# Kernel tuning notes

Measured on AMD Instinct MI355X. Metric: run time of the kernel, lower is better.

## Reference

```python
import jax, jax.numpy as jnp
import numpy as np

N_IN = 1024
N_OUT = 1024
BATCH = 8192
N_GRID = 10  # grid_points = linspace(-1, 1, 10); 9 segments
LN_EPS = 1e-5


def setup_inputs() -> dict:
    key = jax.random.key(0)
    k = jax.random.split(key, 6)
    return {
        "x": jax.random.normal(k[0], (BATCH, N_IN), dtype=jnp.float32),
        "weights": jax.random.normal(k[1], (N_OUT, N_IN), dtype=jnp.float32) * (1.0 / np.sqrt(N_IN)),
        "biases": jax.random.normal(k[2], (N_OUT,), dtype=jnp.float32),
        "slopes": jax.random.normal(k[3], (N_OUT, N_IN, N_GRID - 1), dtype=jnp.float32) * 0.05,
        "intercepts": jax.random.normal(k[4], (N_OUT, N_IN, N_GRID - 1), dtype=jnp.float32) * 0.05,
        "prelu_weight": jnp.full((1,), 0.25, dtype=jnp.float32),
    }


def reference(x, weights, biases, slopes, intercepts, prelu_weight):
    grid = jnp.linspace(-1.0, 1.0, N_GRID, dtype=x.dtype)
    n_seg = N_GRID - 1

    # base branch: GELU (exact, matching torch nn.GELU default) then linear
    b_out = jax.nn.gelu(x, approximate=False) @ weights.T + biases  # [B, n_out]

    # segment index per (sample, input feature)
    pos = (x[..., None] - grid) >= 0  # [B, n_in, N_GRID]
    seg = jnp.clip(jnp.sum(pos.astype(jnp.int32), axis=-1) - 1, 0, n_seg - 1)  # [B, n_in]

    # Faithful to torch.gather semantics: only slopes[:, 0, :] / intercepts[:, 0, :]
    # are read (index dim-2 has size 1 -> j==0). The piecewise sum over n_in then
    # reduces to segment-sums of x and segment counts contracted with those slices.
    onehot = jax.nn.one_hot(seg, n_seg, dtype=x.dtype)  # [B, n_in, n_seg]
    seg_x = jnp.einsum('bis,bi->bs', onehot, x)          # sum of x per segment
    seg_cnt = jnp.sum(onehot, axis=1)                    # count per segment
    slopes0 = slopes[:, 0, :]        # [n_out, n_seg]
    icpt0 = intercepts[:, 0, :]      # [n_out, n_seg]
    lin = seg_x @ slopes0.T + seg_cnt @ icpt0.T          # [B, n_out]

    y = b_out + lin
    # LayerNorm over n_out, no affine
    mu = jnp.mean(y, axis=-1, keepdims=True)
    var = jnp.mean(jnp.square(y - mu), axis=-1, keepdims=True)
    yn = (y - mu) * jax.lax.rsqrt(var + LN_EPS)
    # PReLU with single shared weight
    return jnp.where(yn >= 0, yn, prelu_weight * yn)
```

## Files before the change

### kernel.cpp

```cpp
#include <hip/hip_runtime.h>
#include <hip/hip_fp8.h>

#define N_IN 1024
#define N_OUT 1024
#define BATCHN 8192

typedef __attribute__((ext_vector_type(4))) int intx4;
typedef __attribute__((ext_vector_type(8))) int intx8;
typedef __attribute__((ext_vector_type(16))) float floatx16;

__device__ __forceinline__ unsigned short f2bf(float f) {
  unsigned int u = __float_as_uint(f);
  u += 0x7FFFu + ((u >> 16) & 1u);
  return (unsigned short)(u >> 16);
}
__device__ __forceinline__ float bf2f(unsigned short s) {
  return __uint_as_float(((unsigned int)s) << 16);
}
__device__ __forceinline__ unsigned int f2e4m3(float f) {
  __hip_fp8_e4m3 v(f);
  return (unsigned int)v.__x;
}

__global__ __launch_bounds__(256) void prep_all(const float* __restrict__ x,
                                                unsigned char* __restrict__ g8,
                                                float* __restrict__ seg,
                                                const float* __restrict__ W,
                                                unsigned char* __restrict__ Wb8,
                                                const float* __restrict__ slopes,
                                                const float* __restrict__ icpts,
                                                float* __restrict__ slt,
                                                float* __restrict__ ict) {
  const int b = blockIdx.x;
  const int t = threadIdx.x;
  if (b < BATCHN / 4) {
    const int lane = t & 63, wv = t >> 6;
    const int row = b * 4 + wv;
    const float* xr = x + row * N_IN;
    unsigned int* gr = (unsigned int*)(g8 + row * N_IN);
    float cum[8], cumx[8], totx = 0.f;
#pragma unroll
    for (int s = 0; s < 8; ++s) { cum[s] = 0.f; cumx[s] = 0.f; }
#pragma unroll
    for (int j = 0; j < 4; ++j) {
      float4 v4 = ((const float4*)xr)[lane + 64 * j];
      float vs[4] = {v4.x, v4.y, v4.z, v4.w};
      unsigned int pk = 0;
#pragma unroll
      for (int e = 0; e < 4; ++e) {
        float v = vs[e];
        float gl = 0.5f * v * (1.0f + erff(v * 0.70710678f));
        pk |= f2e4m3(gl * 4.0f) << (8 * e);
        totx += v;
#pragma unroll
        for (int k = 0; k < 8; ++k) {
          bool m = v >= (-1.0f + (float)(k + 1) * (2.0f / 9.0f));
          cum[k] += m ? 1.0f : 0.0f;
          cumx[k] += m ? v : 0.0f;
        }
      }
      gr[lane + 64 * j] = pk;
    }
#pragma unroll
    for (int off = 32; off > 0; off >>= 1) {
      totx += __shfl_xor(totx, off);
#pragma unroll
      for (int s = 0; s < 8; ++s) {
        cum[s] += __shfl_xor(cum[s], off);
        cumx[s] += __shfl_xor(cumx[s], off);
      }
    }
    if (lane == 0) {
      float sx[9], sc[9];
      sx[0] = totx - cumx[0];
      sc[0] = 1024.f - cum[0];
#pragma unroll
      for (int s = 1; s < 8; ++s) {
        sx[s] = cumx[s - 1] - cumx[s];
        sc[s] = cum[s - 1] - cum[s];
      }
      sx[8] = cumx[7];
      sc[8] = cum[7];
#pragma unroll
      for (int s = 0; s < 9; ++s) {
        seg[row * 18 + s] = sx[s];
        seg[row * 18 + 9 + s] = sc[s];
      }
    }
  } else if (b < BATCHN / 4 + N_OUT) {
    const int o = b - BATCHN / 4;
    float4 v = ((const float4*)(W + o * N_IN))[t];
    unsigned int pk = f2e4m3(v.x * 16.0f) | (f2e4m3(v.y * 16.0f) << 8) |
                      (f2e4m3(v.z * 16.0f) << 16) | (f2e4m3(v.w * 16.0f) << 24);
    ((unsigned int*)(Wb8 + o * N_IN))[t] = pk;
  } else {
    const int gb = b - (BATCHN / 4 + N_OUT);
    const int o = gb * 16 + (t >> 4);
    const int s = t & 15;
    if (s < 9) {
      slt[s * N_OUT + o] = slopes[(long)o * 9216 + s];
      ict[s * N_OUT + o] = icpts[(long)o * 9216 + s];
    }
  }
}

#define ASYNC_CP16(gp, lp)                                                     \
  __builtin_amdgcn_global_load_lds(                                            \
      (const __attribute__((address_space(1))) unsigned int*)(gp),             \
      (__attribute__((address_space(3))) unsigned int*)(lp), 16, 0, 0)

__global__ __launch_bounds__(256) void gemm_bt(const unsigned char* __restrict__ A,
                                               const unsigned char* __restrict__ B,
                                               unsigned short* __restrict__ Cb) {
  __shared__ unsigned char lA[128 * 128];
  __shared__ unsigned char lB[128 * 128];
  const int t = threadIdx.x;
  const int m0 = blockIdx.x * 128;
  const int n0 = blockIdx.y * 128;
  const int lane = t & 63, wv = t >> 6;
  const int wm = (wv >> 1) * 64, wn = (wv & 1) * 64;
  floatx16 acc[2][2] = {};

  const int l31 = lane & 31;
  const int lh = lane >> 5;

  for (int kt = 0; kt < N_IN / 128; ++kt) {
    __syncthreads();
    const int ko = kt * 128;
#pragma unroll
    for (int j = 0; j < 4; ++j) {
      const int sg = t + 256 * j;
      const int r = sg >> 3;
      const int lc = (sg & 7) ^ (r & 7);
      ASYNC_CP16(A + (m0 + r) * N_IN + ko + lc * 16, &lA[sg * 16]);
    }
#pragma unroll
    for (int j = 0; j < 4; ++j) {
      const int sg = t + 256 * j;
      const int r = sg >> 3;
      const int lc = (sg & 7) ^ (r & 7);
      ASYNC_CP16(B + (n0 + r) * N_IN + ko + lc * 16, &lB[sg * 16]);
    }
    __syncthreads();
#pragma unroll
    for (int kk = 0; kk < 2; ++kk) {
      const int lc0 = kk * 4 + lh * 2;
      intx8 af[2], bf[2];
#pragma unroll
      for (int i = 0; i < 2; ++i) {
        const int row = wm + i * 32 + l31;
        const int sw = row & 7;
        intx4 lo = *(const intx4*)&lA[row * 128 + ((lc0 ^ sw) * 16)];
        intx4 hi = *(const intx4*)&lA[row * 128 + (((lc0 + 1) ^ sw) * 16)];
        af[i][0] = lo[0]; af[i][1] = lo[1]; af[i][2] = lo[2]; af[i][3] = lo[3];
        af[i][4] = hi[0]; af[i][5] = hi[1]; af[i][6] = hi[2]; af[i][7] = hi[3];
      }
#pragma unroll
      for (int i = 0; i < 2; ++i) {
        const int row = wn + i * 32 + l31;
        const int sw = row & 7;
        intx4 lo = *(const intx4*)&lB[row * 128 + ((lc0 ^ sw) * 16)];
        intx4 hi = *(const intx4*)&lB[row * 128 + (((lc0 + 1) ^ sw) * 16)];
        bf[i][0] = lo[0]; bf[i][1] = lo[1]; bf[i][2] = lo[2]; bf[i][3] = lo[3];
        bf[i][4] = hi[0]; bf[i][5] = hi[1]; bf[i][6] = hi[2]; bf[i][7] = hi[3];
      }
#pragma unroll
      for (int mi = 0; mi < 2; ++mi)
#pragma unroll
        for (int ni = 0; ni < 2; ++ni)
          acc[mi][ni] = __builtin_amdgcn_mfma_scale_f32_32x32x64_f8f6f4(
              af[mi], bf[ni], acc[mi][ni], 0 , 0 ,
              0, 0x7D7D7D7Du , 0, 0x7B7B7B7Bu );
    }
  }

  const int lrow = 4 * lh;
#pragma unroll
  for (int mi = 0; mi < 2; ++mi)
#pragma unroll
    for (int ni = 0; ni < 2; ++ni)
#pragma unroll
      for (int rg = 0; rg < 16; ++rg) {
        const int r = m0 + wm + mi * 32 + (rg & 3) + 8 * (rg >> 2) + lrow;
        const int c = n0 + wn + ni * 32 + l31;
        Cb[r * N_OUT + c] = f2bf(acc[mi][ni][rg]);
      }
}

__global__ __launch_bounds__(512) void ln_prelu(const unsigned short* __restrict__ Cb,
                                                float* __restrict__ out,
                                                const float* __restrict__ biases,
                                                const float* __restrict__ seg,
                                                const float* __restrict__ slt,
                                                const float* __restrict__ ict,
                                                const float* __restrict__ prelu_w) {
  const int t = threadIdx.x;
  const int o = 2 * t;
  const int lane = t & 63, wv = t >> 6;
  const float b1 = biases[o], b2 = biases[o + 1];
  float sl1[9], sl2[9], ic1[9], ic2[9];
#pragma unroll
  for (int s = 0; s < 9; ++s) {
    sl1[s] = slt[s * N_OUT + o];
    sl2[s] = slt[s * N_OUT + o + 1];
    ic1[s] = ict[s * N_OUT + o];
    ic2[s] = ict[s * N_OUT + o + 1];
  }
  const float pw = prelu_w[0];
  __shared__ float2 red[2][8];
  for (int r = 0; r < 8; ++r) {
    const int row = blockIdx.x * 8 + r;
    const float* segr = seg + row * 18;
    ushort2 cc = *(const ushort2*)&Cb[row * N_OUT + o];
    float y1 = bf2f(cc.x) + b1;
    float y2 = bf2f(cc.y) + b2;
#pragma unroll
    for (int s = 0; s < 9; ++s) {
      float sx = segr[s], ct = segr[9 + s];
      y1 += sx * sl1[s] + ct * ic1[s];
      y2 += sx * sl2[s] + ct * ic2[s];
    }
    float sum = y1 + y2;
    float sq = y1 * y1 + y2 * y2;
#pragma unroll
    for (int off = 32; off > 0; off >>= 1) {
      sum += __shfl_xor(sum, off);
      sq += __shfl_xor(sq, off);
    }
    if (lane == 0) red[r & 1][wv] = make_float2(sum, sq);
    __syncthreads();
    float s8 = 0.f, q8 = 0.f;
#pragma unroll
    for (int i = 0; i < 8; ++i) {
      s8 += red[r & 1][i].x;
      q8 += red[r & 1][i].y;
    }
    const float mu = s8 * (1.0f / 1024.0f);
    const float var = q8 * (1.0f / 1024.0f) - mu * mu;
    const float rstd = rsqrtf(var + 1e-5f);
    float z1 = (y1 - mu) * rstd, z2 = (y2 - mu) * rstd;
    z1 = z1 >= 0.f ? z1 : pw * z1;
    z2 = z2 >= 0.f ? z2 : pw * z2;
    *(float2*)&out[row * N_OUT + o] = make_float2(z1, z2);
  }
}

extern "C" void kernel_launch(void* const* d_in, const int* in_sizes, int n_in,
                              void* d_out, int out_size, void* d_ws, size_t ws_size,
                              hipStream_t stream) {
  const float* x = (const float*)d_in[0];
  const float* W = (const float*)d_in[1];
  const float* biases = (const float*)d_in[2];
  const float* slopes = (const float*)d_in[3];
  const float* icpts = (const float*)d_in[4];
  const float* prelu_w = (const float*)d_in[5];
  float* out = (float*)d_out;

  char* ws = (char*)d_ws;
  unsigned char* g8 = (unsigned char*)ws;
  unsigned char* Wb8 = (unsigned char*)(ws + (8u << 20));
  unsigned short* Cb = (unsigned short*)(ws + (16u << 20));
  float* seg = (float*)(ws + (33u << 20));
  float* slt = (float*)(ws + (34u << 20));
  float* ict = (float*)(ws + (34u << 20) + (64u << 10));

  prep_all<<<BATCHN / 4 + N_OUT + 64, 256, 0, stream>>>(x, g8, seg, W, Wb8, slopes,
                                                        icpts, slt, ict);
  gemm_bt<<<dim3(BATCHN / 128, N_OUT / 128), 256, 0, stream>>>(g8, Wb8, Cb);
  ln_prelu<<<BATCHN / 8, 512, 0, stream>>>(Cb, out, biases, seg, slt, ict, prelu_w);
}
```

Before: 175.8 us.

## Use sigmoid GELU approximation and process two rows per LN iteration

Replaces exact erf-based GELU in the prep kernel with a sigmoid approximation x*sigmoid(1.702x) built from fast exp2 and reciprocal intrinsics. It also vectorizes the bias/slope/intercept loads, handles two rows per loop iteration in the LayerNorm/PReLU kernel to halve barriers and add ILP, and uses nontemporal output stores. The GELU approximation adds some error before the already lossy fp8 quantization.

```diff
diff --git a/kernel.cpp b/kernel.cpp
--- a/kernel.cpp
+++ b/kernel.cpp
@@ -8,6 +8,7 @@
 typedef __attribute__((ext_vector_type(4))) int intx4;
 typedef __attribute__((ext_vector_type(8))) int intx8;
 typedef __attribute__((ext_vector_type(16))) float floatx16;
+typedef __attribute__((ext_vector_type(2))) float f32x2;
 
 __device__ __forceinline__ unsigned short f2bf(float f) {
   unsigned int u = __float_as_uint(f);
@@ -20,6 +21,10 @@
 __device__ __forceinline__ unsigned int f2e4m3(float f) {
   __hip_fp8_e4m3 v(f);
   return (unsigned int)v.__x;
+}
+__device__ __forceinline__ float gelu_fast(float v) {
+  float e = __builtin_amdgcn_exp2f(-2.4554443f * v);
+  return v * __builtin_amdgcn_rcpf(1.0f + e);
 }
 
 __global__ __launch_bounds__(256) void prep_all(const float* __restrict__ x,
@@ -49,8 +54,7 @@
 #pragma unroll
       for (int e = 0; e < 4; ++e) {
         float v = vs[e];
-        float gl = 0.5f * v * (1.0f + erff(v * 0.70710678f));
-        pk |= f2e4m3(gl * 4.0f) << (8 * e);
+        pk |= f2e4m3(gelu_fast(v) * 4.0f) << (8 * e);
         totx += v;
 #pragma unroll
         for (int k = 0; k < 8; ++k) {
@@ -197,51 +201,65 @@
   const int t = threadIdx.x;
   const int o = 2 * t;
   const int lane = t & 63, wv = t >> 6;
-  const float b1 = biases[o], b2 = biases[o + 1];
+  const float2 bb = *(const float2*)&biases[o];
   float sl1[9], sl2[9], ic1[9], ic2[9];
 #pragma unroll
   for (int s = 0; s < 9; ++s) {
-    sl1[s] = slt[s * N_OUT + o];
-    sl2[s] = slt[s * N_OUT + o + 1];
-    ic1[s] = ict[s * N_OUT + o];
-    ic2[s] = ict[s * N_OUT + o + 1];
+    float2 sv = *(const float2*)&slt[s * N_OUT + o];
+    float2 iv = *(const float2*)&ict[s * N_OUT + o];
+    sl1[s] = sv.x; sl2[s] = sv.y;
+    ic1[s] = iv.x; ic2[s] = iv.y;
   }
   const float pw = prelu_w[0];
-  __shared__ float2 red[2][8];
-  for (int r = 0; r < 8; ++r) {
-    const int row = blockIdx.x * 8 + r;
-    const float* segr = seg + row * 18;
-    ushort2 cc = *(const ushort2*)&Cb[row * N_OUT + o];
-    float y1 = bf2f(cc.x) + b1;
-    float y2 = bf2f(cc.y) + b2;
+  __shared__ float4 red[2][8];
+  for (int it = 0; it < 4; ++it) {
+    const int rowA = blockIdx.x * 8 + it * 2;
+    const int rowB = rowA + 1;
+    const float* segA = seg + rowA * 18;
+    const float* segB = seg + rowB * 18;
+    ushort2 ca = *(const ushort2*)&Cb[rowA * N_OUT + o];
+    ushort2 cb = *(const ushort2*)&Cb[rowB * N_OUT + o];
+    float ya1 = bf2f(ca.x) + bb.x, ya2 = bf2f(ca.y) + bb.y;
+    float yb1 = bf2f(cb.x) + bb.x, yb2 = bf2f(cb.y) + bb.y;
 #pragma unroll
     for (int s = 0; s < 9; ++s) {
-      float sx = segr[s], ct = segr[9 + s];
-      y1 += sx * sl1[s] + ct * ic1[s];
-      y2 += sx * sl2[s] + ct * ic2[s];
-    }
-    float sum = y1 + y2;
-    float sq = y1 * y1 + y2 * y2;
+      float sxa = segA[s], cta = segA[9 + s];
+      float sxb = segB[s], ctb = segB[9 + s];
+      ya1 += sxa * sl1[s] + cta * ic1[s];
+      ya2 += sxa * sl2[s] + cta * ic2[s];
+      yb1 += sxb * sl1[s] + ctb * ic1[s];
+      yb2 += sxb * sl2[s] + ctb * ic2[s];
+    }
+    float sa = ya1 + ya2, qa = ya1 * ya1 + ya2 * ya2;
+    float sb = yb1 + yb2, qb = yb1 * yb1 + yb2 * yb2;
 #pragma unroll
     for (int off = 32; off > 0; off >>= 1) {
-      sum += __shfl_xor(sum, off);
-      sq += __shfl_xor(sq, off);
-    }
-    if (lane == 0) red[r & 1][wv] = make_float2(sum, sq);
+      sa += __shfl_xor(sa, off);
+      qa += __shfl_xor(qa, off);
+      sb += __shfl_xor(sb, off);
+      qb += __shfl_xor(qb, off);
+    }
+    if (lane == 0) red[it & 1][wv] = make_float4(sa, qa, sb, qb);
     __syncthreads();
-    float s8 = 0.f, q8 = 0.f;
+    float s8a = 0.f, q8a = 0.f, s8b = 0.f, q8b = 0.f;
 #pragma unroll
     for (int i = 0; i < 8; ++i) {
-      s8 += red[r & 1][i].x;
-      q8 += red[r & 1][i].y;
-    }
-    const float mu = s8 * (1.0f / 1024.0f);
-    const float var = q8 * (1.0f / 1024.0f) - mu * mu;
-    const float rstd = rsqrtf(var + 1e-5f);
-    float z1 = (y1 - mu) * rstd, z2 = (y2 - mu) * rstd;
-    z1 = z1 >= 0.f ? z1 : pw * z1;
-    z2 = z2 >= 0.f ? z2 : pw * z2;
-    *(float2*)&out[row * N_OUT + o] = make_float2(z1, z2);
+      float4 p = red[it & 1][i];
+      s8a += p.x; q8a += p.y; s8b += p.z; q8b += p.w;
+    }
+    const float muA = s8a * (1.0f / 1024.0f);
+    const float rstdA = rsqrtf(q8a * (1.0f / 1024.0f) - muA * muA + 1e-5f);
+    const float muB = s8b * (1.0f / 1024.0f);
+    const float rstdB = rsqrtf(q8b * (1.0f / 1024.0f) - muB * muB + 1e-5f);
+    float za1 = (ya1 - muA) * rstdA, za2 = (ya2 - muA) * rstdA;
+    float zb1 = (yb1 - muB) * rstdB, zb2 = (yb2 - muB) * rstdB;
+    za1 = za1 >= 0.f ? za1 : pw * za1;
+    za2 = za2 >= 0.f ? za2 : pw * za2;
+    zb1 = zb1 >= 0.f ? zb1 : pw * zb1;
+    zb2 = zb2 >= 0.f ? zb2 : pw * zb2;
+    f32x2 va = {za1, za2}, vb = {zb1, zb2};
+    __builtin_nontemporal_store(va, (f32x2*)&out[rowA * N_OUT + o]);
+    __builtin_nontemporal_store(vb, (f32x2*)&out[rowB * N_OUT + o]);
   }
 }
 
```

After: 166.6 us. -5.2%, faster.
